# Kernel optimization log

Hardware: AMD Instinct MI355X
Metric: run time of the kernel (lower is better)

The kernel has to match this reference:

```python
import jax, jax.numpy as jnp
import numpy as np

NOISE = 0.1
B, CI, CO, NS, NPTS = 2, 64, 64, 16, 1024
P = B * NS * NPTS  # total per-point noise draws = 32768


def setup_inputs() -> dict:
    key = jax.random.key(0)
    k1, k2, k3, k4 = jax.random.split(key, 4)
    x = jax.random.normal(k1, (B, CI, NS, NPTS), dtype=jnp.float32)
    W = jax.random.normal(k2, (CO, CI), dtype=jnp.float32) * 0.05  # conv.weight[:, :, 0, 0]
    b = jax.random.normal(k3, (CO,), dtype=jnp.float32) * 0.05    # conv.bias (never noised)
    eps = jax.random.normal(k4, (P, CO, CI), dtype=jnp.float32)   # randn_like(weight) per point
    return {"x": x, "W": W, "b": b, "eps": eps}


def reference(x, W, b, eps):
    Bn, Ci, ns, npts = x.shape
    # Faithful to torch: x.reshape(1, in_features, 1, -1) on a [B,Ci,ns,np] tensor
    # (row-major flatten then re-chunk by Ci, which interleaves batch into points).
    xf = x.reshape(Ci, -1)  # [Ci, P]
    # per-point noised weight: W_p = W * (1 + NOISE * eps[p]); bias is shared, un-noised
    base = jnp.einsum('oi,ip->op', W, xf)                      # [CO, P]
    noisy = NOISE * jnp.einsum('poi,oi,ip->op', eps, W, xf)    # [CO, P]
    y = base + noisy + b[:, None]
    return y.reshape(Bn, CO, ns, npts)
```

## Files before the change

kernel.cpp:

```cpp
#include <hip/hip_runtime.h>
#include <cstddef>

constexpr int P_TOTAL = 32768;
constexpr int NCH     = 64;
constexpr int PPB     = 32;
constexpr int PAD     = 68;

__global__ void noise_conv_kernel(const float* __restrict__ x,
                                  const float* __restrict__ W,
                                  const float* __restrict__ bias,
                                  const float* __restrict__ eps,
                                  float* __restrict__ out) {
    __shared__ __align__(16) float t_tile[PPB][PAD];

    const int tid  = threadIdx.x;
    const int p0   = blockIdx.x * PPB;
    const int lane = tid & 63;
    const int wave = tid >> 6;

#pragma unroll
    for (int c = 0; c < (PPB * NCH) / 256; ++c) {
        int e = c * 256 + tid;
        int i = e >> 5;
        int j = e & (PPB - 1);
        t_tile[j][i] = x[i * P_TOTAL + p0 + j];
    }

    float4 wrow[16];
    const float4* wp = reinterpret_cast<const float4*>(W + lane * NCH);
#pragma unroll
    for (int k = 0; k < 16; ++k) wrow[k] = wp[k];
    const float bo = bias[lane];

    __syncthreads();

    for (int r = 0; r < PPB / 4; ++r) {
        const int jr = wave * (PPB / 4) + r;
        const int p  = p0 + jr;
        const float4* ep =
            reinterpret_cast<const float4*>(eps + (size_t)p * (NCH * NCH) + lane * NCH);
        const float4* tp = reinterpret_cast<const float4*>(&t_tile[jr][0]);

        float4 acc = make_float4(0.f, 0.f, 0.f, 0.f);
#pragma unroll
        for (int k = 0; k < 16; ++k) {
            float4 e4 = ep[k];
            float4 t4 = tp[k];
            float4 w4 = wrow[k];
            acc.x = fmaf(w4.x * t4.x, fmaf(0.1f, e4.x, 1.f), acc.x);
            acc.y = fmaf(w4.y * t4.y, fmaf(0.1f, e4.y, 1.f), acc.y);
            acc.z = fmaf(w4.z * t4.z, fmaf(0.1f, e4.z, 1.f), acc.z);
            acc.w = fmaf(w4.w * t4.w, fmaf(0.1f, e4.w, 1.f), acc.w);
        }
        out[(size_t)lane * P_TOTAL + p] = (acc.x + acc.y) + (acc.z + acc.w) + bo;
    }
}

extern "C" void kernel_launch(void* const* d_in, const int* in_sizes, int n_in,
                              void* d_out, int out_size, void* d_ws, size_t ws_size,
                              hipStream_t stream) {
    const float* x    = (const float*)d_in[0];
    const float* W    = (const float*)d_in[1];
    const float* bias = (const float*)d_in[2];
    const float* eps  = (const float*)d_in[3];
    float* out        = (float*)d_out;

    dim3 grid(P_TOTAL / PPB);
    dim3 block(256);
    noise_conv_kernel<<<grid, block, 0, stream>>>(x, W, bias, eps, out);
}
```

Measured before the change: 793.4 us.

## Coalesce eps loads across lanes and reduce partial sums with butterfly shuffles

Each lane now reads consecutive float4 chunks of the per-point eps matrix, so a wave's global loads are fully contiguous. Before, each lane streamed its own 256-byte row, which gave strided accesses. Because a lane no longer owns a whole output row, partial dot products are combined with a transpose-style xor-shuffle reduction. W now lives in shared memory instead of per-thread registers. The kernel is bound by streaming eps (512 MB), so better coalescing is the main lever; the cost is extra shuffle and LDS instructions.

Measured after the change: 693.4 us. -12.6%, faster.

```diff
diff --git a/kernel.cpp b/kernel.cpp
--- a/kernel.cpp
+++ b/kernel.cpp
@@ -4,55 +4,99 @@
 constexpr int P_TOTAL = 32768;
 constexpr int NCH     = 64;
 constexpr int PPB     = 32;
-constexpr int PAD     = 68;
+constexpr int PPW     = 8;
+constexpr int XPAD    = 68;
 
-__global__ void noise_conv_kernel(const float* __restrict__ x,
-                                  const float* __restrict__ W,
-                                  const float* __restrict__ bias,
-                                  const float* __restrict__ eps,
-                                  float* __restrict__ out) {
-    __shared__ __align__(16) float t_tile[PPB][PAD];
+__global__ __launch_bounds__(256) void noise_conv_kernel(
+    const float* __restrict__ x, const float* __restrict__ W,
+    const float* __restrict__ bias, const float* __restrict__ eps,
+    float* __restrict__ out)
+{
+    __shared__ __align__(16) float4 Wl[NCH * NCH / 4];
+    __shared__ __align__(16) float  xt[PPB][XPAD];
 
     const int tid  = threadIdx.x;
+    const int lane = tid & 63;
+    const int wv   = tid >> 6;
     const int p0   = blockIdx.x * PPB;
-    const int lane = tid & 63;
-    const int wave = tid >> 6;
+    const int g    = lane >> 4;
+    const int s    = lane & 15;
 
+    const float4* W4 = reinterpret_cast<const float4*>(W);
+#pragma unroll
+    for (int c = 0; c < 4; ++c) {
+        int idx = c * 256 + tid;
+        Wl[idx] = W4[idx];
+    }
 #pragma unroll
     for (int c = 0; c < (PPB * NCH) / 256; ++c) {
         int e = c * 256 + tid;
         int i = e >> 5;
         int j = e & (PPB - 1);
-        t_tile[j][i] = x[i * P_TOTAL + p0 + j];
+        xt[j][i] = x[i * P_TOTAL + p0 + j];
     }
 
-    float4 wrow[16];
-    const float4* wp = reinterpret_cast<const float4*>(W + lane * NCH);
-#pragma unroll
-    for (int k = 0; k < 16; ++k) wrow[k] = wp[k];
-    const float bo = bias[lane];
+    const int   o_fin = 4 * s + g;
+    const float b_fin = bias[o_fin];
 
     __syncthreads();
 
-    for (int r = 0; r < PPB / 4; ++r) {
-        const int jr = wave * (PPB / 4) + r;
-        const int p  = p0 + jr;
-        const float4* ep =
-            reinterpret_cast<const float4*>(eps + (size_t)p * (NCH * NCH) + lane * NCH);
-        const float4* tp = reinterpret_cast<const float4*>(&t_tile[jr][0]);
+    for (int j = 0; j < PPW; ++j) {
+        const int jj = wv * PPW + j;
+        const int p  = p0 + jj;
+        const float4* ep4 = reinterpret_cast<const float4*>(eps)
+                          + (size_t)p * (NCH * NCH / 4) + lane;
 
-        float4 acc = make_float4(0.f, 0.f, 0.f, 0.f);
+        float4 e[16];
+#pragma unroll
+        for (int k = 0; k < 16; ++k) e[k] = ep4[k * 64];
+
+        const float4 x4 = *reinterpret_cast<const float4*>(&xt[jj][4 * s]);
+
+        float acc[16];
 #pragma unroll
         for (int k = 0; k < 16; ++k) {
-            float4 e4 = ep[k];
-            float4 t4 = tp[k];
-            float4 w4 = wrow[k];
-            acc.x = fmaf(w4.x * t4.x, fmaf(0.1f, e4.x, 1.f), acc.x);
-            acc.y = fmaf(w4.y * t4.y, fmaf(0.1f, e4.y, 1.f), acc.y);
-            acc.z = fmaf(w4.z * t4.z, fmaf(0.1f, e4.z, 1.f), acc.z);
-            acc.w = fmaf(w4.w * t4.w, fmaf(0.1f, e4.w, 1.f), acc.w);
+            float4 w4 = Wl[k * 64 + lane];
+            float wx0 = w4.x * x4.x, wx1 = w4.y * x4.y;
+            float wx2 = w4.z * x4.z, wx3 = w4.w * x4.w;
+            float f0 = fmaf(0.1f, e[k].x, 1.0f);
+            float f1 = fmaf(0.1f, e[k].y, 1.0f);
+            float f2 = fmaf(0.1f, e[k].z, 1.0f);
+            float f3 = fmaf(0.1f, e[k].w, 1.0f);
+            float a  = wx0 * f0;
+            a = fmaf(wx1, f1, a);
+            a = fmaf(wx2, f2, a);
+            a = fmaf(wx3, f3, a);
+            acc[k] = a;
         }
-        out[(size_t)lane * P_TOTAL + p] = (acc.x + acc.y) + (acc.z + acc.w) + bo;
+
+        float r8[8];
+#pragma unroll
+        for (int t = 0; t < 8; ++t) {
+            float mine  = (s & 8) ? acc[t + 8] : acc[t];
+            float other = (s & 8) ? acc[t]     : acc[t + 8];
+            r8[t] = mine + __shfl_xor(other, 8, 64);
+        }
+        float r4[4];
+#pragma unroll
+        for (int t = 0; t < 4; ++t) {
+            float mine  = (s & 4) ? r8[t + 4] : r8[t];
+            float other = (s & 4) ? r8[t]     : r8[t + 4];
+            r4[t] = mine + __shfl_xor(other, 4, 64);
+        }
+        float r2[2];
+#pragma unroll
+        for (int t = 0; t < 2; ++t) {
+            float mine  = (s & 2) ? r4[t + 2] : r4[t];
+            float other = (s & 2) ? r4[t]     : r4[t + 2];
+            r2[t] = mine + __shfl_xor(other, 2, 64);
+        }
+        {
+            float mine  = (s & 1) ? r2[1] : r2[0];
+            float other = (s & 1) ? r2[0] : r2[1];
+            float y = mine + __shfl_xor(other, 1, 64) + b_fin;
+            out[(size_t)o_fin * P_TOTAL + p] = y;
+        }
     }
 }
 
```
